# Kernel optimization log

Measured on AMD Instinct MI355X. Metric: run time of the kernel, lower is better.

The kernel has to match this reference:

```python
import jax, jax.numpy as jnp
import numpy as np

N = 100000   # nodes
E = 1600000  # edges (avg degree 16)
DIN = 128
DH = 64


def setup_inputs() -> dict:
    key = jax.random.key(0)
    ks = jax.random.split(key, 6)
    x = jax.random.normal(ks[0], (N, DIN), dtype=jnp.float32)
    edge_index = jax.random.randint(ks[1], (2, E), 0, N, dtype=jnp.int32)
    W1 = jax.random.normal(ks[2], (DIN, DH), dtype=jnp.float32) * (1.0 / np.sqrt(DIN))
    b1 = jnp.zeros((DH,), dtype=jnp.float32)
    W2 = jax.random.normal(ks[3], (DH, DH), dtype=jnp.float32) * (1.0 / np.sqrt(DH))
    b2 = jnp.zeros((DH,), dtype=jnp.float32)
    alpha = jnp.full((DH,), 0.25, dtype=jnp.float32)  # PReLU per-channel slope (torch default 0.25)
    return {"x": x, "edge_index": edge_index, "W1": W1, "b1": b1, "W2": W2, "b2": b2, "alpha": alpha}


def _gcn_layer(h, src, dst, norm, W, b):
    # GCNConv: linear transform, then normalized scatter-add aggregation, then bias
    h = h @ W                                  # [N, dout]
    msg = h[src] * norm[:, None]               # [E+N, dout] gathered + scaled messages
    agg = jax.ops.segment_sum(msg, dst, num_segments=N)
    return agg + b


def reference(x, edge_index, W1, b1, W2, b2, alpha):
    src0, dst0 = edge_index[0], edge_index[1]
    # GCNConv default: add self-loops, symmetric normalization deg^{-1/2} A deg^{-1/2}
    loops = jnp.arange(N, dtype=src0.dtype)
    src = jnp.concatenate([src0, loops])
    dst = jnp.concatenate([dst0, loops])
    ones = jnp.ones(src.shape[0], dtype=x.dtype)
    deg = jax.ops.segment_sum(ones, dst, num_segments=N)
    dinv = jnp.where(deg > 0, jax.lax.rsqrt(deg), 0.0)
    norm = dinv[src] * dinv[dst]               # [E+N]

    prelu = lambda z: jnp.where(z >= 0, z, alpha * z)  # shared per-channel PReLU
    z = prelu(_gcn_layer(x, src, dst, norm, W1, b1))
    z = prelu(_gcn_layer(z, src, dst, norm, W2, b2))
    return z
```

## Files before the change

### kernel.cpp

```cpp
#include <hip/hip_runtime.h>
#include <hip/hip_bf16.h>

#define NN 100000
#define NE 1600000
#define NBUCK 391
#define CAP 5120

typedef __attribute__((ext_vector_type(8))) short short8;
typedef __attribute__((ext_vector_type(4))) float f32x4;

static __device__ __forceinline__ unsigned short f2bf(float f) {
    unsigned u = __float_as_uint(f);
    unsigned r = (u + 0x7fffu + ((u >> 16) & 1u)) >> 16;
    return (unsigned short)r;
}
static __device__ __forceinline__ float bf_lo(unsigned u) {
    return __uint_as_float(u << 16);
}
static __device__ __forceinline__ float bf_hi(unsigned u) {
    return __uint_as_float(u & 0xffff0000u);
}
static __device__ __forceinline__ void acc8(float* acc, uint4 v, float nm) {
    acc[0] += bf_lo(v.x) * nm; acc[1] += bf_hi(v.x) * nm;
    acc[2] += bf_lo(v.y) * nm; acc[3] += bf_hi(v.y) * nm;
    acc[4] += bf_lo(v.z) * nm; acc[5] += bf_hi(v.z) * nm;
    acc[6] += bf_lo(v.w) * nm; acc[7] += bf_hi(v.w) * nm;
}

#define CHUNK 2048
__global__ __launch_bounds__(256) void k_partition(const int* __restrict__ ei,
                                                   int* __restrict__ bcur,
                                                   unsigned* __restrict__ ebuf) {
    __shared__ int lh[NBUCK];
    __shared__ int lbase[NBUCK];
    int tid = threadIdx.x;
    int e0 = blockIdx.x * CHUNK;
    for (int i = tid; i < NBUCK; i += 256) lh[i] = 0;
    __syncthreads();
    #pragma unroll
    for (int k = 0; k < CHUNK; k += 256) {
        int e = e0 + k + tid;
        if (e < NE) atomicAdd(&lh[ei[NE + e] >> 8], 1);
    }
    __syncthreads();
    for (int i = tid; i < NBUCK; i += 256) {
        int c = lh[i];
        lbase[i] = c ? atomicAdd(&bcur[i], c) : 0;
        lh[i] = 0;
    }
    __syncthreads();
    #pragma unroll
    for (int k = 0; k < CHUNK; k += 256) {
        int e = e0 + k + tid;
        if (e < NE) {
            int d = ei[NE + e];
            int s = ei[e];
            int b = d >> 8;
            int r = atomicAdd(&lh[b], 1);
            int pos = lbase[b] + r;
            if (pos < CAP)
                ebuf[(long)b * CAP + pos] = ((unsigned)s << 8) | (unsigned)(d & 255);
        }
    }
}

__global__ __launch_bounds__(256) void k_build(const int* __restrict__ bcur,
                                               const unsigned* __restrict__ ebuf,
                                               unsigned* __restrict__ rowinfo,
                                               float* __restrict__ dinv,
                                               int* __restrict__ esrc) {
    __shared__ int cnt[256];
    __shared__ int wsum[4];
    int tid = threadIdx.x;
    int base = blockIdx.x * CAP;
    int nedge = bcur[blockIdx.x];
    if (nedge > CAP) nedge = CAP;
    cnt[tid] = 0;
    __syncthreads();
    for (int j = tid; j < nedge; j += 256)
        atomicAdd(&cnt[ebuf[base + j] & 255u], 1);
    __syncthreads();
    int v = cnt[tid];
    int lane = tid & 63;
    int incl = v;
    #pragma unroll
    for (int off = 1; off < 64; off <<= 1) {
        int t = __shfl_up(incl, off, 64);
        if (lane >= off) incl += t;
    }
    if (lane == 63) wsum[tid >> 6] = incl;
    __syncthreads();
    if (tid == 0) {
        int a = 0;
        #pragma unroll
        for (int w = 0; w < 4; ++w) { int t = wsum[w]; wsum[w] = a; a += t; }
    }
    __syncthreads();
    int ex = incl - v + wsum[tid >> 6];
    int node = blockIdx.x * 256 + tid;
    if (node < NN) {
        rowinfo[node] = ((unsigned)(base + ex) << 11) | (unsigned)v;
        dinv[node] = rsqrtf((float)(v + 1));
    }
    cnt[tid] = base + ex;
    __syncthreads();
    for (int j = tid; j < nedge; j += 256) {
        unsigned p = ebuf[base + j];
        int pos = atomicAdd(&cnt[p & 255u], 1);
        esrc[pos] = (int)(p >> 8);
    }
}

template <int K, bool BF16IN>
__global__ __launch_bounds__(256) void k_mm(const void* __restrict__ in_,
                                            const float* __restrict__ W,
                                            unsigned short* __restrict__ hout) {
    constexpr int KP = K + 8;
    __shared__ unsigned short Wt[64 * KP];
    int tid = threadIdx.x;
    for (int idx = tid; idx < K * 64; idx += 256) {
        int k = idx >> 6, n = idx & 63;
        Wt[n * KP + k] = f2bf(W[idx]);
    }
    __syncthreads();

    int wave = tid >> 6, lane = tid & 63;
    int m = lane & 15, q = lane >> 4;
    int n0 = blockIdx.x * 64 + wave * 16;

    f32x4 acc[4] = {{0.f,0.f,0.f,0.f},{0.f,0.f,0.f,0.f},{0.f,0.f,0.f,0.f},{0.f,0.f,0.f,0.f}};
    int row = n0 + m;
    int rowc = row < NN ? row : NN - 1;

    #pragma unroll
    for (int kk = 0; kk < K / 32; ++kk) {
        short8 afrag;
        if (BF16IN) {
            const unsigned short* xr = (const unsigned short*)in_ + (long)rowc * K;
            afrag = *(const short8*)(xr + kk * 32 + q * 8);
        } else {
            const float* xr = (const float*)in_ + (long)rowc * K;
            const float4* p = (const float4*)(xr + kk * 32 + q * 8);
            float4 v0 = p[0], v1 = p[1];
            float xv[8] = {v0.x, v0.y, v0.z, v0.w, v1.x, v1.y, v1.z, v1.w};
            #pragma unroll
            for (int i2 = 0; i2 < 8; ++i2) afrag[i2] = (short)f2bf(xv[i2]);
        }
        #pragma unroll
        for (int nt = 0; nt < 4; ++nt) {
            const short8* bp = (const short8*)&Wt[(nt * 16 + m) * KP + kk * 32 + q * 8];
            acc[nt] = __builtin_amdgcn_mfma_f32_16x16x32_bf16(afrag, *bp, acc[nt], 0, 0, 0);
        }
    }

    #pragma unroll
    for (int reg = 0; reg < 4; ++reg) {
        int node = n0 + q * 4 + reg;
        if (node < NN) {
            #pragma unroll
            for (int nt = 0; nt < 4; ++nt)
                hout[(long)node * 64 + nt * 16 + m] = f2bf(acc[nt][reg]);
        }
    }
}

template <bool OUT_BF16>
__global__ __launch_bounds__(256) void k_agg(const unsigned* __restrict__ rowinfo,
                                             const int* __restrict__ esrc,
                                             const unsigned short* __restrict__ h,
                                             const float* __restrict__ dinv,
                                             const float* __restrict__ bias,
                                             const float* __restrict__ alpha,
                                             void* __restrict__ out_) {
    int sl = threadIdx.x & 7;
    int node = blockIdx.x * 32 + (threadIdx.x >> 3);
    if (node >= NN) return;
    unsigned u = rowinfo[node];
    int start = (int)(u >> 11);
    int cnt = (int)(u & 2047u);
    float dn = dinv[node];
    const unsigned short* hc = h + sl * 8;

    float acc[8];
    {
        uint4 hw = *(const uint4*)(hc + (long)node * 64);
        float d2 = dn * dn;
        acc[0] = bf_lo(hw.x) * d2; acc[1] = bf_hi(hw.x) * d2;
        acc[2] = bf_lo(hw.y) * d2; acc[3] = bf_hi(hw.y) * d2;
        acc[4] = bf_lo(hw.z) * d2; acc[5] = bf_hi(hw.z) * d2;
        acc[6] = bf_lo(hw.w) * d2; acc[7] = bf_hi(hw.w) * d2;
    }

    int i = 0;
    for (; i + 4 <= cnt; i += 4) {
        int s0 = esrc[start + i];
        int s1 = esrc[start + i + 1];
        int s2 = esrc[start + i + 2];
        int s3 = esrc[start + i + 3];
        float n0 = dinv[s0] * dn, n1 = dinv[s1] * dn;
        float n2 = dinv[s2] * dn, n3 = dinv[s3] * dn;
        uint4 w0 = *(const uint4*)(hc + (long)s0 * 64);
        uint4 w1 = *(const uint4*)(hc + (long)s1 * 64);
        uint4 w2 = *(const uint4*)(hc + (long)s2 * 64);
        uint4 w3 = *(const uint4*)(hc + (long)s3 * 64);
        acc8(acc, w0, n0); acc8(acc, w1, n1); acc8(acc, w2, n2); acc8(acc, w3, n3);
    }
    for (; i < cnt; ++i) {
        int s0 = esrc[start + i];
        float n0 = dinv[s0] * dn;
        uint4 w0 = *(const uint4*)(hc + (long)s0 * 64);
        acc8(acc, w0, n0);
    }

    float4 blo = *(const float4*)(bias + sl * 8);
    float4 bhi = *(const float4*)(bias + sl * 8 + 4);
    float4 alo = *(const float4*)(alpha + sl * 8);
    float4 ahi = *(const float4*)(alpha + sl * 8 + 4);
    float bb[8] = {blo.x, blo.y, blo.z, blo.w, bhi.x, bhi.y, bhi.z, bhi.w};
    float aa[8] = {alo.x, alo.y, alo.z, alo.w, ahi.x, ahi.y, ahi.z, ahi.w};
    #pragma unroll
    for (int j = 0; j < 8; ++j) {
        float v = acc[j] + bb[j];
        acc[j] = v >= 0.f ? v : aa[j] * v;
    }

    if (OUT_BF16) {
        uint4 pk;
        pk.x = (unsigned)f2bf(acc[0]) | ((unsigned)f2bf(acc[1]) << 16);
        pk.y = (unsigned)f2bf(acc[2]) | ((unsigned)f2bf(acc[3]) << 16);
        pk.z = (unsigned)f2bf(acc[4]) | ((unsigned)f2bf(acc[5]) << 16);
        pk.w = (unsigned)f2bf(acc[6]) | ((unsigned)f2bf(acc[7]) << 16);
        *(uint4*)((unsigned short*)out_ + (long)node * 64 + sl * 8) = pk;
    } else {
        float* op = (float*)out_ + (long)node * 64 + sl * 8;
        *(float4*)op = make_float4(acc[0], acc[1], acc[2], acc[3]);
        *(float4*)(op + 4) = make_float4(acc[4], acc[5], acc[6], acc[7]);
    }
}

extern "C" void kernel_launch(void* const* d_in, const int* in_sizes, int n_in,
                              void* d_out, int out_size, void* d_ws, size_t ws_size,
                              hipStream_t stream) {
    const float* x     = (const float*)d_in[0];
    const int*   ei    = (const int*)d_in[1];
    const float* W1    = (const float*)d_in[2];
    const float* b1    = (const float*)d_in[3];
    const float* W2    = (const float*)d_in[4];
    const float* b2    = (const float*)d_in[5];
    const float* alpha = (const float*)d_in[6];
    float* out = (float*)d_out;

    char* ws = (char*)d_ws;
    float*    dinv      = (float*)(ws);
    unsigned* rowinfo   = (unsigned*)(ws + 400384);
    int*      bcur      = (int*)(ws + 800768);
    int*      esrc      = (int*)(ws + 802816);
    unsigned short* hbf = (unsigned short*)(ws + 8810496);
    unsigned* ebuf      = (unsigned*)(ws + 21610496);
    unsigned short* aggbf = (unsigned short*)(ws + 21610496);

    (void)hipMemsetAsync(bcur, 0, NBUCK * sizeof(int), stream);
    k_partition<<<(NE + CHUNK - 1) / CHUNK, 256, 0, stream>>>(ei, bcur, ebuf);
    k_build<<<NBUCK, 256, 0, stream>>>(bcur, ebuf, rowinfo, dinv, esrc);

    k_mm<128, false><<<(NN + 63) / 64, 256, 0, stream>>>(x, W1, hbf);
    k_agg<true><<<(NN + 31) / 32, 256, 0, stream>>>(rowinfo, esrc, hbf, dinv, b1, alpha, aggbf);
    k_mm<64, true><<<(NN + 63) / 64, 256, 0, stream>>>(aggbf, W2, hbf);
    k_agg<false><<<(NN + 31) / 32, 256, 0, stream>>>(rowinfo, esrc, hbf, dinv, b2, alpha, out);
}
```

Before: 238.6 us.

## Merge edge partition with first GEMM and pack source dinv into edge list

Edge partitioning and the first-layer x@W1 GEMM now run as two block ranges of one launch, so these independent stages can overlap. Degrees come from global atomics into a new deg array, and a separate small kernel turns them into dinv. k_build now writes (src, dinv[src]) pairs, so aggregation gets the normalisation from the same load instead of a random dinv gather, and the node's own dinv is recomputed from its count. In exchange it adds 1.6M global atomics, one more launch, and doubles the bytes of the edge array that each aggregation reads.

```diff
diff --git a/kernel.cpp b/kernel.cpp
--- a/kernel.cpp
+++ b/kernel.cpp
@@ -5,6 +5,9 @@
 #define NE 1600000
 #define NBUCK 391
 #define CAP 5120
+#define CHUNK 2048
+#define PBLOCKS 782
+#define MMBLOCKS 1563
 
 typedef __attribute__((ext_vector_type(8))) short short8;
 typedef __attribute__((ext_vector_type(4))) float f32x4;
@@ -27,48 +30,104 @@
     acc[6] += bf_lo(v.w) * nm; acc[7] += bf_hi(v.w) * nm;
 }
 
-#define CHUNK 2048
-__global__ __launch_bounds__(256) void k_partition(const int* __restrict__ ei,
-                                                   int* __restrict__ bcur,
-                                                   unsigned* __restrict__ ebuf) {
-    __shared__ int lh[NBUCK];
-    __shared__ int lbase[NBUCK];
+__global__ __launch_bounds__(256) void k_fat(const int* __restrict__ ei,
+                                             int* __restrict__ bcur,
+                                             unsigned* __restrict__ ebuf,
+                                             int* __restrict__ deg,
+                                             const float* __restrict__ x,
+                                             const float* __restrict__ W1,
+                                             unsigned short* __restrict__ hout) {
+    __shared__ unsigned char smem[17408];
     int tid = threadIdx.x;
-    int e0 = blockIdx.x * CHUNK;
-    for (int i = tid; i < NBUCK; i += 256) lh[i] = 0;
-    __syncthreads();
-    #pragma unroll
-    for (int k = 0; k < CHUNK; k += 256) {
-        int e = e0 + k + tid;
-        if (e < NE) atomicAdd(&lh[ei[NE + e] >> 8], 1);
-    }
-    __syncthreads();
-    for (int i = tid; i < NBUCK; i += 256) {
-        int c = lh[i];
-        lbase[i] = c ? atomicAdd(&bcur[i], c) : 0;
-        lh[i] = 0;
-    }
-    __syncthreads();
-    #pragma unroll
-    for (int k = 0; k < CHUNK; k += 256) {
-        int e = e0 + k + tid;
-        if (e < NE) {
-            int d = ei[NE + e];
-            int s = ei[e];
-            int b = d >> 8;
-            int r = atomicAdd(&lh[b], 1);
-            int pos = lbase[b] + r;
-            if (pos < CAP)
-                ebuf[(long)b * CAP + pos] = ((unsigned)s << 8) | (unsigned)(d & 255);
-        }
+    if (blockIdx.x < PBLOCKS) {
+        int* lh = (int*)smem;
+        int* lbase = lh + NBUCK;
+        int e0 = blockIdx.x * CHUNK;
+        for (int i = tid; i < NBUCK; i += 256) lh[i] = 0;
+        __syncthreads();
+        #pragma unroll
+        for (int k = 0; k < CHUNK; k += 256) {
+            int e = e0 + k + tid;
+            if (e < NE) {
+                int d = ei[NE + e];
+                atomicAdd(&lh[d >> 8], 1);
+                atomicAdd(&deg[d], 1);
+            }
+        }
+        __syncthreads();
+        for (int i = tid; i < NBUCK; i += 256) {
+            int c = lh[i];
+            lbase[i] = c ? atomicAdd(&bcur[i], c) : 0;
+            lh[i] = 0;
+        }
+        __syncthreads();
+        #pragma unroll
+        for (int k = 0; k < CHUNK; k += 256) {
+            int e = e0 + k + tid;
+            if (e < NE) {
+                int d = ei[NE + e];
+                int s = ei[e];
+                int b = d >> 8;
+                int r = atomicAdd(&lh[b], 1);
+                int pos = lbase[b] + r;
+                if (pos < CAP)
+                    ebuf[(long)b * CAP + pos] = ((unsigned)s << 8) | (unsigned)(d & 255);
+            }
+        }
+    } else {
+        constexpr int K = 128, KP = K + 8;
+        unsigned short* Wt = (unsigned short*)smem;
+        for (int idx = tid; idx < K * 64; idx += 256) {
+            int k = idx >> 6, n = idx & 63;
+            Wt[n * KP + k] = f2bf(W1[idx]);
+        }
+        __syncthreads();
+        int wave = tid >> 6, lane = tid & 63;
+        int m = lane & 15, q = lane >> 4;
+        int n0 = (blockIdx.x - PBLOCKS) * 64 + wave * 16;
+        f32x4 acc[4] = {{0.f,0.f,0.f,0.f},{0.f,0.f,0.f,0.f},{0.f,0.f,0.f,0.f},{0.f,0.f,0.f,0.f}};
+        int row = n0 + m;
+        int rowc = row < NN ? row : NN - 1;
+        const float* xr = x + (long)rowc * K;
+        #pragma unroll
+        for (int kk = 0; kk < K / 32; ++kk) {
+            const float4* p = (const float4*)(xr + kk * 32 + q * 8);
+            float4 v0 = p[0], v1 = p[1];
+            float xv[8] = {v0.x, v0.y, v0.z, v0.w, v1.x, v1.y, v1.z, v1.w};
+            short8 afrag;
+            #pragma unroll
+            for (int i2 = 0; i2 < 8; ++i2) afrag[i2] = (short)f2bf(xv[i2]);
+            #pragma unroll
+            for (int nt = 0; nt < 4; ++nt) {
+                const short8* bp = (const short8*)&Wt[(nt * 16 + m) * KP + kk * 32 + q * 8];
+                acc[nt] = __builtin_amdgcn_mfma_f32_16x16x32_bf16(afrag, *bp, acc[nt], 0, 0, 0);
+            }
+        }
+        #pragma unroll
+        for (int reg = 0; reg < 4; ++reg) {
+            int node = n0 + q * 4 + reg;
+            if (node < NN) {
+                #pragma unroll
+                for (int nt = 0; nt < 4; ++nt)
+                    hout[(long)node * 64 + nt * 16 + m] = f2bf(acc[nt][reg]);
+            }
+        }
+    }
+}
+
+__global__ __launch_bounds__(256) void k_dinv(int* __restrict__ deg) {
+    int i = blockIdx.x * 256 + threadIdx.x;
+    if (i < NN) {
+        float dv = rsqrtf((float)deg[i] + 1.0f);
+        ((float*)deg)[i] = dv;
     }
 }
 
 __global__ __launch_bounds__(256) void k_build(const int* __restrict__ bcur,
                                                const unsigned* __restrict__ ebuf,
+                                               const float* __restrict__ dinv,
                                                unsigned* __restrict__ rowinfo,
-                                               float* __restrict__ dinv,
-                                               int* __restrict__ esrc) {
+                                               int2* __restrict__ epair) {
     __shared__ int cnt[256];
     __shared__ int wsum[4];
     int tid = threadIdx.x;
@@ -98,24 +157,22 @@
     __syncthreads();
     int ex = incl - v + wsum[tid >> 6];
     int node = blockIdx.x * 256 + tid;
-    if (node < NN) {
+    if (node < NN)
         rowinfo[node] = ((unsigned)(base + ex) << 11) | (unsigned)v;
-        dinv[node] = rsqrtf((float)(v + 1));
-    }
     cnt[tid] = base + ex;
     __syncthreads();
     for (int j = tid; j < nedge; j += 256) {
         unsigned p = ebuf[base + j];
+        int s = (int)(p >> 8);
         int pos = atomicAdd(&cnt[p & 255u], 1);
-        esrc[pos] = (int)(p >> 8);
-    }
-}
-
-template <int K, bool BF16IN>
-__global__ __launch_bounds__(256) void k_mm(const void* __restrict__ in_,
-                                            const float* __restrict__ W,
-                                            unsigned short* __restrict__ hout) {
-    constexpr int KP = K + 8;
+        epair[pos] = make_int2(s, __float_as_int(dinv[s]));
+    }
+}
+
+__global__ __launch_bounds__(256) void k_mm64(const unsigned short* __restrict__ in_,
+                                              const float* __restrict__ W,
+                                              unsigned short* __restrict__ hout) {
+    constexpr int K = 64, KP = K + 8;
     __shared__ unsigned short Wt[64 * KP];
     int tid = threadIdx.x;
     for (int idx = tid; idx < K * 64; idx += 256) {
@@ -123,36 +180,22 @@
         Wt[n * KP + k] = f2bf(W[idx]);
     }
     __syncthreads();
-
     int wave = tid >> 6, lane = tid & 63;
     int m = lane & 15, q = lane >> 4;
     int n0 = blockIdx.x * 64 + wave * 16;
-
     f32x4 acc[4] = {{0.f,0.f,0.f,0.f},{0.f,0.f,0.f,0.f},{0.f,0.f,0.f,0.f},{0.f,0.f,0.f,0.f}};
     int row = n0 + m;
     int rowc = row < NN ? row : NN - 1;
-
+    const unsigned short* xr = in_ + (long)rowc * K;
     #pragma unroll
     for (int kk = 0; kk < K / 32; ++kk) {
-        short8 afrag;
-        if (BF16IN) {
-            const unsigned short* xr = (const unsigned short*)in_ + (long)rowc * K;
-            afrag = *(const short8*)(xr + kk * 32 + q * 8);
-        } else {
-            const float* xr = (const float*)in_ + (long)rowc * K;
-            const float4* p = (const float4*)(xr + kk * 32 + q * 8);
-            float4 v0 = p[0], v1 = p[1];
-            float xv[8] = {v0.x, v0.y, v0.z, v0.w, v1.x, v1.y, v1.z, v1.w};
-            #pragma unroll
-            for (int i2 = 0; i2 < 8; ++i2) afrag[i2] = (short)f2bf(xv[i2]);
-        }
+        short8 afrag = *(const short8*)(xr + kk * 32 + q * 8);
         #pragma unroll
         for (int nt = 0; nt < 4; ++nt) {
             const short8* bp = (const short8*)&Wt[(nt * 16 + m) * KP + kk * 32 + q * 8];
             acc[nt] = __builtin_amdgcn_mfma_f32_16x16x32_bf16(afrag, *bp, acc[nt], 0, 0, 0);
         }
     }
-
     #pragma unroll
     for (int reg = 0; reg < 4; ++reg) {
         int node = n0 + q * 4 + reg;
@@ -166,9 +209,8 @@
 
 template <bool OUT_BF16>
 __global__ __launch_bounds__(256) void k_agg(const unsigned* __restrict__ rowinfo,
-                                             const int* __restrict__ esrc,
+                                             const int2* __restrict__ epair,
                                              const unsigned short* __restrict__ h,
-                                             const float* __restrict__ dinv,
                                              const float* __restrict__ bias,
                                              const float* __restrict__ alpha,
                                              void* __restrict__ out_) {
@@ -178,7 +220,7 @@
     unsigned u = rowinfo[node];
     int start = (int)(u >> 11);
     int cnt = (int)(u & 2047u);
-    float dn = dinv[node];
+    float dn = rsqrtf((float)cnt + 1.0f);
     const unsigned short* hc = h + sl * 8;
 
     float acc[8];
@@ -193,22 +235,22 @@
 
     int i = 0;
     for (; i + 4 <= cnt; i += 4) {
-        int s0 = esrc[start + i];
-        int s1 = esrc[start + i + 1];
-        int s2 = esrc[start + i + 2];
-        int s3 = esrc[start + i + 3];
-        float n0 = dinv[s0] * dn, n1 = dinv[s1] * dn;
-        float n2 = dinv[s2] * dn, n3 = dinv[s3] * dn;
-        uint4 w0 = *(const uint4*)(hc + (long)s0 * 64);
-        uint4 w1 = *(const uint4*)(hc + (long)s1 * 64);
-        uint4 w2 = *(const uint4*)(hc + (long)s2 * 64);
-        uint4 w3 = *(const uint4*)(hc + (long)s3 * 64);
+        int2 p0 = epair[start + i];
+        int2 p1 = epair[start + i + 1];
+        int2 p2 = epair[start + i + 2];
+        int2 p3 = epair[start + i + 3];
+        float n0 = __int_as_float(p0.y) * dn, n1 = __int_as_float(p1.y) * dn;
+        float n2 = __int_as_float(p2.y) * dn, n3 = __int_as_float(p3.y) * dn;
+        uint4 w0 = *(const uint4*)(hc + (long)p0.x * 64);
+        uint4 w1 = *(const uint4*)(hc + (long)p1.x * 64);
+        uint4 w2 = *(const uint4*)(hc + (long)p2.x * 64);
+        uint4 w3 = *(const uint4*)(hc + (long)p3.x * 64);
         acc8(acc, w0, n0); acc8(acc, w1, n1); acc8(acc, w2, n2); acc8(acc, w3, n3);
     }
     for (; i < cnt; ++i) {
-        int s0 = esrc[start + i];
-        float n0 = dinv[s0] * dn;
-        uint4 w0 = *(const uint4*)(hc + (long)s0 * 64);
+        int2 p0 = epair[start + i];
+        float n0 = __int_as_float(p0.y) * dn;
+        uint4 w0 = *(const uint4*)(hc + (long)p0.x * 64);
         acc8(acc, w0, n0);
     }
 
@@ -251,20 +293,20 @@
     float* out = (float*)d_out;
 
     char* ws = (char*)d_ws;
-    float*    dinv      = (float*)(ws);
-    unsigned* rowinfo   = (unsigned*)(ws + 400384);
-    int*      bcur      = (int*)(ws + 800768);
-    int*      esrc      = (int*)(ws + 802816);
-    unsigned short* hbf = (unsigned short*)(ws + 8810496);
-    unsigned* ebuf      = (unsigned*)(ws + 21610496);
-    unsigned short* aggbf = (unsigned short*)(ws + 21610496);
-
-    (void)hipMemsetAsync(bcur, 0, NBUCK * sizeof(int), stream);
-    k_partition<<<(NE + CHUNK - 1) / CHUNK, 256, 0, stream>>>(ei, bcur, ebuf);
-    k_build<<<NBUCK, 256, 0, stream>>>(bcur, ebuf, rowinfo, dinv, esrc);
-
-    k_mm<128, false><<<(NN + 63) / 64, 256, 0, stream>>>(x, W1, hbf);
-    k_agg<true><<<(NN + 31) / 32, 256, 0, stream>>>(rowinfo, esrc, hbf, dinv, b1, alpha, aggbf);
-    k_mm<64, true><<<(NN + 63) / 64, 256, 0, stream>>>(aggbf, W2, hbf);
-    k_agg<false><<<(NN + 31) / 32, 256, 0, stream>>>(rowinfo, esrc, hbf, dinv, b2, alpha, out);
-}
+    int*      deg       = (int*)(ws);
+    int*      bcur      = (int*)(ws + 400384);
+    unsigned* rowinfo   = (unsigned*)(ws + 402432);
+    int2*     epair     = (int2*)(ws + 802816);
+    unsigned short* hbf = (unsigned short*)(ws + 16818176);
+    unsigned* ebuf      = (unsigned*)(ws + 29618176);
+    unsigned short* aggbf = (unsigned short*)(ws + 29618176);
+
+    (void)hipMemsetAsync(deg, 0, 402432, stream);
+    k_fat<<<PBLOCKS + MMBLOCKS, 256, 0, stream>>>(ei, bcur, ebuf, deg, x, W1, hbf);
+    k_dinv<<<391, 256, 0, stream>>>(deg);
+    k_build<<<NBUCK, 256, 0, stream>>>(bcur, ebuf, (const float*)deg, rowinfo, epair);
+
+    k_agg<true><<<(NN + 31) / 32, 256, 0, stream>>>(rowinfo, epair, hbf, b1, alpha, aggbf);
+    k_mm64<<<(NN + 63) / 64, 256, 0, stream>>>(aggbf, W2, hbf);
+    k_agg<false><<<(NN + 31) / 32, 256, 0, stream>>>(rowinfo, epair, hbf, b2, alpha, out);
+}
```

Result: slower. 294.8 us (+23.5%).

## Merge edge partition and first matmul into one launch; unroll aggregation by eight

Applied to the files above, without the earlier changes.

Edge partitioning and the first-layer dense transform are independent, so both now run as one launch. Blocks below a fixed index do the partition and the rest do the x@W1 MFMA tile, which removes one kernel launch and lets the two phases share the GPU. The aggregation loop now issues eight neighbour gathers per iteration instead of four, keeping more memory loads in flight. The cost is a larger shared-memory footprint for the merged kernel and more registers in the aggregation kernel.

```diff
diff --git a/kernel.cpp b/kernel.cpp
--- a/kernel.cpp
+++ b/kernel.cpp
@@ -5,6 +5,9 @@
 #define NE 1600000
 #define NBUCK 391
 #define CAP 5120
+#define CHUNK 2048
+#define PBLOCKS 782
+#define MMBLOCKS 1563
 
 typedef __attribute__((ext_vector_type(8))) short short8;
 typedef __attribute__((ext_vector_type(4))) float f32x4;
@@ -27,39 +30,82 @@
     acc[6] += bf_lo(v.w) * nm; acc[7] += bf_hi(v.w) * nm;
 }
 
-#define CHUNK 2048
-__global__ __launch_bounds__(256) void k_partition(const int* __restrict__ ei,
-                                                   int* __restrict__ bcur,
-                                                   unsigned* __restrict__ ebuf) {
-    __shared__ int lh[NBUCK];
-    __shared__ int lbase[NBUCK];
+__global__ __launch_bounds__(256) void k_fat(const int* __restrict__ ei,
+                                             int* __restrict__ bcur,
+                                             unsigned* __restrict__ ebuf,
+                                             const float* __restrict__ x,
+                                             const float* __restrict__ W1,
+                                             unsigned short* __restrict__ hout) {
+    __shared__ __attribute__((aligned(16))) unsigned char smem[17408];
     int tid = threadIdx.x;
-    int e0 = blockIdx.x * CHUNK;
-    for (int i = tid; i < NBUCK; i += 256) lh[i] = 0;
-    __syncthreads();
-    #pragma unroll
-    for (int k = 0; k < CHUNK; k += 256) {
-        int e = e0 + k + tid;
-        if (e < NE) atomicAdd(&lh[ei[NE + e] >> 8], 1);
-    }
-    __syncthreads();
-    for (int i = tid; i < NBUCK; i += 256) {
-        int c = lh[i];
-        lbase[i] = c ? atomicAdd(&bcur[i], c) : 0;
-        lh[i] = 0;
-    }
-    __syncthreads();
-    #pragma unroll
-    for (int k = 0; k < CHUNK; k += 256) {
-        int e = e0 + k + tid;
-        if (e < NE) {
-            int d = ei[NE + e];
-            int s = ei[e];
-            int b = d >> 8;
-            int r = atomicAdd(&lh[b], 1);
-            int pos = lbase[b] + r;
-            if (pos < CAP)
-                ebuf[(long)b * CAP + pos] = ((unsigned)s << 8) | (unsigned)(d & 255);
+    if (blockIdx.x < PBLOCKS) {
+        int* lh = (int*)smem;
+        int* lbase = lh + NBUCK;
+        int e0 = blockIdx.x * CHUNK;
+        for (int i = tid; i < NBUCK; i += 256) lh[i] = 0;
+        __syncthreads();
+        #pragma unroll
+        for (int k = 0; k < CHUNK; k += 256) {
+            int e = e0 + k + tid;
+            if (e < NE) atomicAdd(&lh[ei[NE + e] >> 8], 1);
+        }
+        __syncthreads();
+        for (int i = tid; i < NBUCK; i += 256) {
+            int c = lh[i];
+            lbase[i] = c ? atomicAdd(&bcur[i], c) : 0;
+            lh[i] = 0;
+        }
+        __syncthreads();
+        #pragma unroll
+        for (int k = 0; k < CHUNK; k += 256) {
+            int e = e0 + k + tid;
+            if (e < NE) {
+                int d = ei[NE + e];
+                int s = ei[e];
+                int b = d >> 8;
+                int r = atomicAdd(&lh[b], 1);
+                int pos = lbase[b] + r;
+                if (pos < CAP)
+                    ebuf[(long)b * CAP + pos] = ((unsigned)s << 8) | (unsigned)(d & 255);
+            }
+        }
+    } else {
+        constexpr int K = 128, KP = K + 8;
+        unsigned short* Wt = (unsigned short*)smem;
+        for (int idx = tid; idx < K * 64; idx += 256) {
+            int k = idx >> 6, n = idx & 63;
+            Wt[n * KP + k] = f2bf(W1[idx]);
+        }
+        __syncthreads();
+        int wave = tid >> 6, lane = tid & 63;
+        int m = lane & 15, q = lane >> 4;
+        int n0 = (blockIdx.x - PBLOCKS) * 64 + wave * 16;
+        f32x4 acc[4] = {{0.f,0.f,0.f,0.f},{0.f,0.f,0.f,0.f},{0.f,0.f,0.f,0.f},{0.f,0.f,0.f,0.f}};
+        int row = n0 + m;
+        int rowc = row < NN ? row : NN - 1;
+        const float* xr = x + (long)rowc * K;
+        #pragma unroll
+        for (int kk = 0; kk < K / 32; ++kk) {
+            const float4* p = (const float4*)(xr + kk * 32 + q * 8);
+            float4 v0 = p[0], v1 = p[1];
+            float xv[8] = {v0.x, v0.y, v0.z, v0.w, v1.x, v1.y, v1.z, v1.w};
+            short8 afrag;
+            #pragma unroll
+            for (int i2 = 0; i2 < 8; ++i2) afrag[i2] = (short)f2bf(xv[i2]);
+            #pragma unroll
+            for (int nt = 0; nt < 4; ++nt) {
+                const short8* bp = (const short8*)&Wt[(nt * 16 + m) * KP + kk * 32 + q * 8];
+                acc[nt] = __builtin_amdgcn_mfma_f32_16x16x32_bf16(afrag, *bp, acc[nt], 0, 0, 0);
+            }
+        }
+        #pragma unroll
+        for (int reg = 0; reg < 4; ++reg) {
+            int node = n0 + q * 4 + reg;
+            if (node < NN) {
+                #pragma unroll
+                for (int nt = 0; nt < 4; ++nt)
+                    hout[(long)node * 64 + nt * 16 + m] = f2bf(acc[nt][reg]);
+            }
         }
     }
 }
@@ -111,11 +157,10 @@
     }
 }
 
-template <int K, bool BF16IN>
-__global__ __launch_bounds__(256) void k_mm(const void* __restrict__ in_,
-                                            const float* __restrict__ W,
-                                            unsigned short* __restrict__ hout) {
-    constexpr int KP = K + 8;
+__global__ __launch_bounds__(256) void k_mm64(const unsigned short* __restrict__ in_,
+                                              const float* __restrict__ W,
+                                              unsigned short* __restrict__ hout) {
+    constexpr int K = 64, KP = K + 8;
     __shared__ unsigned short Wt[64 * KP];
     int tid = threadIdx.x;
     for (int idx = tid; idx < K * 64; idx += 256) {
@@ -123,36 +168,22 @@
         Wt[n * KP + k] = f2bf(W[idx]);
     }
     __syncthreads();
-
     int wave = tid >> 6, lane = tid & 63;
     int m = lane & 15, q = lane >> 4;
     int n0 = blockIdx.x * 64 + wave * 16;
-
     f32x4 acc[4] = {{0.f,0.f,0.f,0.f},{0.f,0.f,0.f,0.f},{0.f,0.f,0.f,0.f},{0.f,0.f,0.f,0.f}};
     int row = n0 + m;
     int rowc = row < NN ? row : NN - 1;
-
+    const unsigned short* xr = in_ + (long)rowc * K;
     #pragma unroll
     for (int kk = 0; kk < K / 32; ++kk) {
-        short8 afrag;
-        if (BF16IN) {
-            const unsigned short* xr = (const unsigned short*)in_ + (long)rowc * K;
-            afrag = *(const short8*)(xr + kk * 32 + q * 8);
-        } else {
-            const float* xr = (const float*)in_ + (long)rowc * K;
-            const float4* p = (const float4*)(xr + kk * 32 + q * 8);
-            float4 v0 = p[0], v1 = p[1];
-            float xv[8] = {v0.x, v0.y, v0.z, v0.w, v1.x, v1.y, v1.z, v1.w};
-            #pragma unroll
-            for (int i2 = 0; i2 < 8; ++i2) afrag[i2] = (short)f2bf(xv[i2]);
-        }
+        short8 afrag = *(const short8*)(xr + kk * 32 + q * 8);
         #pragma unroll
         for (int nt = 0; nt < 4; ++nt) {
             const short8* bp = (const short8*)&Wt[(nt * 16 + m) * KP + kk * 32 + q * 8];
             acc[nt] = __builtin_amdgcn_mfma_f32_16x16x32_bf16(afrag, *bp, acc[nt], 0, 0, 0);
         }
     }
-
     #pragma unroll
     for (int reg = 0; reg < 4; ++reg) {
         int node = n0 + q * 4 + reg;
@@ -192,7 +223,31 @@
     }
 
     int i = 0;
-    for (; i + 4 <= cnt; i += 4) {
+    for (; i + 8 <= cnt; i += 8) {
+        int s0 = esrc[start + i];
+        int s1 = esrc[start + i + 1];
+        int s2 = esrc[start + i + 2];
+        int s3 = esrc[start + i + 3];
+        int s4 = esrc[start + i + 4];
+        int s5 = esrc[start + i + 5];
+        int s6 = esrc[start + i + 6];
+        int s7 = esrc[start + i + 7];
+        float n0 = dinv[s0] * dn, n1 = dinv[s1] * dn;
+        float n2 = dinv[s2] * dn, n3 = dinv[s3] * dn;
+        float n4 = dinv[s4] * dn, n5 = dinv[s5] * dn;
+        float n6 = dinv[s6] * dn, n7 = dinv[s7] * dn;
+        uint4 w0 = *(const uint4*)(hc + (long)s0 * 64);
+        uint4 w1 = *(const uint4*)(hc + (long)s1 * 64);
+        uint4 w2 = *(const uint4*)(hc + (long)s2 * 64);
+        uint4 w3 = *(const uint4*)(hc + (long)s3 * 64);
+        uint4 w4 = *(const uint4*)(hc + (long)s4 * 64);
+        uint4 w5 = *(const uint4*)(hc + (long)s5 * 64);
+        uint4 w6 = *(const uint4*)(hc + (long)s6 * 64);
+        uint4 w7 = *(const uint4*)(hc + (long)s7 * 64);
+        acc8(acc, w0, n0); acc8(acc, w1, n1); acc8(acc, w2, n2); acc8(acc, w3, n3);
+        acc8(acc, w4, n4); acc8(acc, w5, n5); acc8(acc, w6, n6); acc8(acc, w7, n7);
+    }
+    if (i + 4 <= cnt) {
         int s0 = esrc[start + i];
         int s1 = esrc[start + i + 1];
         int s2 = esrc[start + i + 2];
@@ -204,6 +259,7 @@
         uint4 w2 = *(const uint4*)(hc + (long)s2 * 64);
         uint4 w3 = *(const uint4*)(hc + (long)s3 * 64);
         acc8(acc, w0, n0); acc8(acc, w1, n1); acc8(acc, w2, n2); acc8(acc, w3, n3);
+        i += 4;
     }
     for (; i < cnt; ++i) {
         int s0 = esrc[start + i];
@@ -260,11 +316,10 @@
     unsigned short* aggbf = (unsigned short*)(ws + 21610496);
 
     (void)hipMemsetAsync(bcur, 0, NBUCK * sizeof(int), stream);
-    k_partition<<<(NE + CHUNK - 1) / CHUNK, 256, 0, stream>>>(ei, bcur, ebuf);
+    k_fat<<<PBLOCKS + MMBLOCKS, 256, 0, stream>>>(ei, bcur, ebuf, x, W1, hbf);
     k_build<<<NBUCK, 256, 0, stream>>>(bcur, ebuf, rowinfo, dinv, esrc);
 
-    k_mm<128, false><<<(NN + 63) / 64, 256, 0, stream>>>(x, W1, hbf);
     k_agg<true><<<(NN + 31) / 32, 256, 0, stream>>>(rowinfo, esrc, hbf, dinv, b1, alpha, aggbf);
-    k_mm<64, true><<<(NN + 63) / 64, 256, 0, stream>>>(aggbf, W2, hbf);
+    k_mm64<<<(NN + 63) / 64, 256, 0, stream>>>(aggbf, W2, hbf);
     k_agg<false><<<(NN + 31) / 32, 256, 0, stream>>>(rowinfo, esrc, hbf, dinv, b2, alpha, out);
 }
```

After: 243.9 us. +2.2%, slower.
